# Kernel optimization log

Measured on AMD Instinct MI355X. Metric: run time of the kernel, lower is better.

Reference implementation:

```python
import jax, jax.numpy as jnp
import numpy as np

EMBED_DIM = 1024
NUM_HEADS = 16
HEAD_DIM = EMBED_DIM // NUM_HEADS  # used only for the softmax scale


def setup_inputs() -> dict:
    key = jax.random.key(0)
    k_x, k_wqkv, k_bqkv, k_wo, k_bo = jax.random.split(key, 5)
    bound_qkv = 1.0 / np.sqrt(EMBED_DIM)
    return {
        "x": jax.random.normal(k_x, (4, 2048, EMBED_DIM), dtype=jnp.float32),
        "W_qkv": jax.random.uniform(k_wqkv, (EMBED_DIM, 3 * EMBED_DIM), jnp.float32, -bound_qkv, bound_qkv),
        "b_qkv": jax.random.uniform(k_bqkv, (3 * EMBED_DIM,), jnp.float32, -bound_qkv, bound_qkv),
        "W_out": jax.random.uniform(k_wo, (EMBED_DIM, EMBED_DIM), jnp.float32, -bound_qkv, bound_qkv),
        "b_out": jax.random.uniform(k_bo, (EMBED_DIM,), jnp.float32, -bound_qkv, bound_qkv),
    }


def reference(x, W_qkv, b_qkv, W_out, b_out):
    # fused QKV projection: [B,S,3E]
    qkv = jnp.einsum("bse,ef->bsf", x, W_qkv) + b_qkv
    q, k, v = jnp.split(qkv, 3, axis=-1)  # each [B,S,E]
    scale = 1.0 / jnp.sqrt(jnp.float32(HEAD_DIM))
    # NOTE: no head reshape — attention over full embed_dim, scale uses head_dim
    scores = jnp.einsum("bqe,bke->bqk", q, k) * scale  # [B,S,S]
    attn = jax.nn.softmax(scores, axis=-1)
    context = jnp.einsum("bqk,bke->bqe", attn, v)  # [B,S,E]
    return jnp.einsum("bse,ef->bsf", context, W_out) + b_out
```

## Files before the change

### kernel.cpp

```cpp
#include <hip/hip_runtime.h>

typedef unsigned short u16;
typedef __bf16   bf16x8 __attribute__((ext_vector_type(8)));
typedef float    f32x4  __attribute__((ext_vector_type(4)));
typedef unsigned short u16x4 __attribute__((ext_vector_type(4)));
typedef unsigned short u16x8 __attribute__((ext_vector_type(8)));

__device__ inline float bf2f(u16 u) { return __uint_as_float(((unsigned int)u) << 16); }
__device__ inline u16 f2bf(float f) {
    unsigned int u = __float_as_uint(f);
    u += 0x7FFF + ((u >> 16) & 1);
    return (u16)(u >> 16);
}

__device__ inline void gl2lds16(const u16* g, u16* l) {
    __builtin_amdgcn_global_load_lds(
        (const __attribute__((address_space(1))) void*)g,
        (__attribute__((address_space(3))) void*)l, 16, 0, 0);
}

__global__ __launch_bounds__(256)
void sniff_zero(const u16* __restrict__ x, int* __restrict__ flag,
                float* __restrict__ sums) {
    sums[blockIdx.x * 256 + threadIdx.x] = 0.0f;
    if (blockIdx.x == 0 && threadIdx.x < 64) {
        const int lane = threadIdx.x;
        const unsigned idx = lane * 131072u + 65536u;
        const u16 u = x[idx];
        const int e = (u >> 7) & 0xFF;
        const unsigned long long b = __ballot(e >= 100 && e <= 140);
        if (lane == 0) flag[0] = (__popcll(b) >= 48) ? 0 : 1;
    }
}

__global__ __launch_bounds__(256)
void convx_biases(const void* __restrict__ x, u16* __restrict__ xbf,
                  const void* __restrict__ b1, const void* __restrict__ b2,
                  u16* __restrict__ o1, u16* __restrict__ o2,
                  const int* __restrict__ flagp) {
    const int f = *flagp;
    if (blockIdx.x < 8192) {
        const long i = ((long)blockIdx.x * 256 + threadIdx.x) * 4;
        if (f) {
            f32x4 v = *(const f32x4*)((const float*)x + i);
            u16x4 o; o[0] = f2bf(v[0]); o[1] = f2bf(v[1]); o[2] = f2bf(v[2]); o[3] = f2bf(v[3]);
            *(u16x4*)(xbf + i) = o;
        } else {
            *(u16x4*)(xbf + i) = *(const u16x4*)((const u16*)x + i);
        }
    } else {
        const int i = (blockIdx.x - 8192) * 256 + threadIdx.x;
        if (i < 3072) o1[i] = f ? f2bf(((const float*)b1)[i]) : ((const u16*)b1)[i];
        else { const int j = i - 3072;
               o2[j] = f ? f2bf(((const float*)b2)[j]) : ((const u16*)b2)[j]; }
    }
}

__global__ __launch_bounds__(256)
void transpose_w(const void* __restrict__ Wqkv, u16* __restrict__ WqkvT,
                 const void* __restrict__ Wout, u16* __restrict__ WoutT,
                 const int* __restrict__ flagp)
{
    const void* in; u16* out; long inStride, outStride;
    if (blockIdx.z == 0) { in = Wqkv; out = WqkvT; inStride = 3072; outStride = 1024; }
    else { if (blockIdx.x >= 32) return;
           in = Wout; out = WoutT; inStride = 1024; outStride = 1024; }
    __shared__ u16 t[32][36];
    const int isF32 = *flagp;
    const int tid = threadIdx.x;
    const long r0 = (long)blockIdx.y * 32;
    const long c0 = (long)blockIdx.x * 32;
    const int r  = tid >> 3;
    const int c4 = (tid & 7) * 4;
    const long base = (r0 + r) * inStride + c0 + c4;
    u16x4 v;
    if (isF32) {
        f32x4 f = *(const f32x4*)((const float*)in + base);
        v[0] = f2bf(f[0]); v[1] = f2bf(f[1]); v[2] = f2bf(f[2]); v[3] = f2bf(f[3]);
    } else {
        v = *(const u16x4*)((const u16*)in + base);
    }
    t[r][c4 + 0] = v[0]; t[r][c4 + 1] = v[1]; t[r][c4 + 2] = v[2]; t[r][c4 + 3] = v[3];
    __syncthreads();
    u16x4 o;
    o[0] = t[c4 + 0][r]; o[1] = t[c4 + 1][r]; o[2] = t[c4 + 2][r]; o[3] = t[c4 + 3][r];
    *(u16x4*)&out[(c0 + r) * outStride + r0 + c4] = o;
}

template <int GM, int GN, int WM, int WN>
__device__ __forceinline__ void kloop(
    const u16* __restrict__ A, const u16* __restrict__ Bt,
    int K, long lda, long ldb, long m0, long n0,
    u16* __restrict__ As, u16* __restrict__ Bs, f32x4 (&acc)[WM][WN])
{
    constexpr int BM = GM * WM * 16;
    constexpr int BN = GN * WN * 16;
    constexpr int IA = BM / 32;
    constexpr int IB = BN / 32;
    const int tid  = threadIdx.x;
    const int lane = tid & 63;
    const int wave = tid >> 6;
    const int sr   = tid >> 3;
    const int qg0  = (tid & 7) ^ (sr & 7);
    const u16* pa[IA]; const u16* pb[IB];
    u16* la[IA]; u16* lb[IB];
#pragma unroll
    for (int i = 0; i < IA; ++i) {
        pa[i] = A + (m0 + i * 32 + sr) * lda + qg0 * 8;
        la[i] = As + (i * 256 + wave * 64) * 8;
    }
#pragma unroll
    for (int i = 0; i < IB; ++i) {
        pb[i] = Bt + (n0 + i * 32 + sr) * ldb + qg0 * 8;
        lb[i] = Bs + (i * 256 + wave * 64) * 8;
    }
    const int wm = (wave / GN) * (WM * 16);
    const int wn = (wave % GN) * (WN * 16);
    const int lr = lane & 15;
    const int hk = lane >> 4;
    int aoff[WM][2], boff[WN][2];
#pragma unroll
    for (int i = 0; i < WM; ++i) {
        const int row = wm + i * 16 + lr, r7 = row & 7;
        aoff[i][0] = row * 64 + ((hk     ^ r7) * 8);
        aoff[i][1] = row * 64 + (((4+hk) ^ r7) * 8);
    }
#pragma unroll
    for (int j = 0; j < WN; ++j) {
        const int row = wn + j * 16 + lr, r7 = row & 7;
        boff[j][0] = row * 64 + ((hk     ^ r7) * 8);
        boff[j][1] = row * 64 + (((4+hk) ^ r7) * 8);
    }
    for (int kt = 0; kt < K; kt += 64) {
#pragma unroll
        for (int i = 0; i < IA; ++i) { gl2lds16(pa[i], la[i]); pa[i] += 64; }
#pragma unroll
        for (int i = 0; i < IB; ++i) { gl2lds16(pb[i], lb[i]); pb[i] += 64; }
        __syncthreads();
#pragma unroll
        for (int ks = 0; ks < 2; ++ks) {
            bf16x8 af[WM], bf[WN];
#pragma unroll
            for (int i = 0; i < WM; ++i) af[i] = *(const bf16x8*)&As[aoff[i][ks]];
#pragma unroll
            for (int j = 0; j < WN; ++j) bf[j] = *(const bf16x8*)&Bs[boff[j][ks]];
#pragma unroll
            for (int i = 0; i < WM; ++i)
#pragma unroll
                for (int j = 0; j < WN; ++j)
                    acc[i][j] = __builtin_amdgcn_mfma_f32_16x16x32_bf16(af[i], bf[j], acc[i][j], 0, 0, 0);
        }
        __syncthreads();
    }
}

template <int WM, int WN, typename F>
__device__ __forceinline__ void epi_bf16(u16* __restrict__ Sw, u16* __restrict__ C,
    long ldc, long gm0, long gn0, int lane, F f)
{
    const int lr = lane & 15, hk = lane >> 4;
#pragma unroll
    for (int i = 0; i < WM; ++i)
#pragma unroll
        for (int j = 0; j < WN; ++j)
#pragma unroll
            for (int r = 0; r < 4; ++r)
                Sw[(i*16 + hk*4 + r) * (WN*16) + j*16 + lr] = f2bf(f(i, j, r));
    asm volatile("s_waitcnt lgkmcnt(0)" ::: "memory");
    constexpr int LPR = WN * 2;
    constexpr int RPI = 64 / LPR;
    const int rl = lane / LPR, c8 = (lane % LPR) * 8;
#pragma unroll
    for (int t = 0; t < (WM*16) / RPI; ++t) {
        const int row = t * RPI + rl;
        u16x8 v8 = *(const u16x8*)&Sw[row * (WN*16) + c8];
        *(u16x8*)&C[(gm0 + row) * ldc + gn0 + c8] = v8;
    }
}

template <int WM, int WN, typename F>
__device__ __forceinline__ void epi_f32(float* __restrict__ Sw, float* __restrict__ C,
    long ldc, long gm0, long gn0, int lane, F f)
{
    const int lr = lane & 15, hk = lane >> 4;
#pragma unroll
    for (int jh = 0; jh < 2; ++jh) {
#pragma unroll
        for (int i = 0; i < WM; ++i)
#pragma unroll
            for (int jj = 0; jj < WN/2; ++jj)
#pragma unroll
                for (int r = 0; r < 4; ++r)
                    Sw[(i*16 + hk*4 + r) * (WN*8) + jj*16 + lr] = f(i, jh*(WN/2) + jj, r);
        asm volatile("s_waitcnt lgkmcnt(0)" ::: "memory");
        constexpr int LPR = WN * 2;
        constexpr int RPI = 64 / LPR;
        const int rl = lane / LPR, c4 = (lane % LPR) * 4;
#pragma unroll
        for (int t = 0; t < (WM*16) / RPI; ++t) {
            const int row = t * RPI + rl;
            f32x4 v4 = *(const f32x4*)&Sw[row * (WN*8) + c4];
            *(f32x4*)&C[(gm0 + row) * ldc + gn0 + jh*(WN*8) + c4] = v4;
        }
        asm volatile("s_waitcnt lgkmcnt(0)" ::: "memory");
    }
}

template<int MH, int NH, typename FI>
__device__ __forceinline__ void phase256(const u16* Ab, const u16* Bb,
    int aB0, int aB1, int bB0, int bB1, f32x4 (&acc)[2][2][4][2], FI issue)
{
    bf16x8 af[2][4], bv[2][2];
#pragma unroll
    for (int i = 0; i < 4; ++i) {
        af[0][i] = *(const bf16x8*)&Ab[aB0 + MH*8192 + i*1024];
        af[1][i] = *(const bf16x8*)&Ab[aB1 + MH*8192 + i*1024];
    }
#pragma unroll
    for (int j = 0; j < 2; ++j) {
        bv[0][j] = *(const bf16x8*)&Bb[bB0 + NH*8192 + j*1024];
        bv[1][j] = *(const bf16x8*)&Bb[bB1 + NH*8192 + j*1024];
    }
    issue();
    __builtin_amdgcn_s_barrier();
    asm volatile("s_waitcnt lgkmcnt(0)" ::: "memory");
    __builtin_amdgcn_s_setprio(1);
#pragma unroll
    for (int ks = 0; ks < 2; ++ks)
#pragma unroll
        for (int i = 0; i < 4; ++i)
#pragma unroll
            for (int j = 0; j < 2; ++j)
                acc[MH][NH][i][j] = __builtin_amdgcn_mfma_f32_16x16x32_bf16(
                    af[ks][i], bv[ks][j], acc[MH][NH][i][j], 0, 0, 0);
    __builtin_amdgcn_s_setprio(0);
}

__device__ __forceinline__ void kloop256(
    const u16* __restrict__ A, const u16* __restrict__ Bt,
    int K, long lda, long ldb, long m0, long n0,
    u16* __restrict__ S, f32x4 (&acc)[2][2][4][2])
{
    constexpr int BUF = 256 * 64;
    const int tid  = threadIdx.x;
    const int wave = tid >> 6, lane = tid & 63;
    const int wmi  = wave >> 2, wni = wave & 3;
    const int sr   = tid >> 3;
    const int qg   = ((tid & 7) ^ (sr & 7)) * 8;
    const int lr   = lane & 15, hk = lane >> 4, l7 = lane & 7;
    const u16* pA = A + (m0 + sr) * lda + qg;
    const u16* pB = Bt + (n0 + sr) * ldb + qg;
    u16* const lA = S + wave * 512;
    u16* const lB = S + 2 * BUF + wave * 512;
    const int aB0 = (wmi*64 + lr)*64 + ((hk       ^ l7) * 8);
    const int aB1 = (wmi*64 + lr)*64 + (((4 + hk) ^ l7) * 8);
    const int bB0 = (wni*32 + lr)*64 + ((hk       ^ l7) * 8);
    const int bB1 = (wni*32 + lr)*64 + (((4 + hk) ^ l7) * 8);
    const int NT = K >> 6;

    auto stA = [&](int buf, int mh, int kt) {
        const u16* s = pA + (long)mh * 128 * lda + kt;
        u16* d = lA + buf * BUF + mh * 8192;
        gl2lds16(s, d);
        gl2lds16(s + 64 * lda, d + 4096);
    };
    auto stB = [&](int buf, int nh, int kt) {
        const u16* s = pB + (long)nh * 128 * ldb + kt;
        u16* d = lB + buf * BUF + nh * 8192;
        gl2lds16(s, d);
        gl2lds16(s + 64 * ldb, d + 4096);
    };

    stA(0, 0, 0); stB(0, 0, 0); stA(0, 1, 0); stB(0, 1, 0);
    stA(1, 0, 64); stB(1, 0, 64);
    asm volatile("s_waitcnt vmcnt(4)" ::: "memory");
    __builtin_amdgcn_s_barrier();

    for (int t = 0; t < NT; ++t) {
        const int b = t & 1;
        const u16* Ab = S + b * BUF;
        const u16* Bb = S + 2 * BUF + b * BUF;
        const int kt = t << 6;
        phase256<0,0>(Ab, Bb, aB0, aB1, bB0, bB1, acc,
                      [&]{ if (t + 1 < NT) stA(b ^ 1, 1, kt + 64); });
        __builtin_amdgcn_s_barrier();
        phase256<0,1>(Ab, Bb, aB0, aB1, bB0, bB1, acc,
                      [&]{ if (t + 1 < NT) stB(b ^ 1, 1, kt + 64); });
        __builtin_amdgcn_s_barrier();
        phase256<1,0>(Ab, Bb, aB0, aB1, bB0, bB1, acc,
                      [&]{ if (t + 2 < NT) stA(b, 0, kt + 128); });
        __builtin_amdgcn_s_barrier();
        phase256<1,1>(Ab, Bb, aB0, aB1, bB0, bB1, acc,
                      [&]{ if (t + 2 < NT) stB(b, 0, kt + 128); });
        if (t + 2 < NT)      asm volatile("s_waitcnt vmcnt(4)" ::: "memory");
        else if (t + 1 < NT) asm volatile("s_waitcnt vmcnt(0)" ::: "memory");
        __builtin_amdgcn_s_barrier();
    }
}

template <typename F>
__device__ __forceinline__ void epi256_bf16(u16* __restrict__ Sw, u16* __restrict__ C,
    long ldc, long m0, long n0, int wmi, int wni, int lane, F f)
{
    const int lr = lane & 15, hk = lane >> 4;
#pragma unroll
    for (int mh = 0; mh < 2; ++mh)
#pragma unroll
    for (int i = 0; i < 4; ++i)
#pragma unroll
    for (int r = 0; r < 4; ++r)
#pragma unroll
    for (int nh = 0; nh < 2; ++nh)
#pragma unroll
    for (int j = 0; j < 2; ++j)
        Sw[(mh*64 + i*16 + hk*4 + r) * 64 + nh*32 + j*16 + lr] = f2bf(f(mh, nh, i, j, r));
    asm volatile("s_waitcnt lgkmcnt(0)" ::: "memory");
    const int rl = lane >> 3, c8 = (lane & 7) * 8;
    const long gcolb = n0 + (long)((c8 >> 5) * 128 + wni * 32 + (c8 & 31));
#pragma unroll
    for (int t = 0; t < 16; ++t) {
        const int row = t * 8 + rl;
        const long grow = m0 + (row >> 6) * 128 + wmi * 64 + (row & 63);
        *(u16x8*)&C[grow * ldc + gcolb] = *(const u16x8*)&Sw[row * 64 + c8];
    }
}

__global__ __launch_bounds__(512, 2)
void gemm_qkv256(const u16* __restrict__ A, const u16* __restrict__ Bt,
                 u16* __restrict__ C, const u16* __restrict__ bias)
{
    __shared__ __align__(16) u16 S[65536];
    const long m0 = (long)blockIdx.y * 256, n0 = (long)blockIdx.x * 256;
    f32x4 acc[2][2][4][2] = {};
    kloop256(A, Bt, 1024, 1024L, 1024L, m0, n0, S, acc);
    const int lane = threadIdx.x & 63, wave = threadIdx.x >> 6;
    const int wmi = wave >> 2, wni = wave & 3;
    const int lr = lane & 15;
    float bj[2][2];
#pragma unroll
    for (int nh = 0; nh < 2; ++nh)
#pragma unroll
        for (int j = 0; j < 2; ++j)
            bj[nh][j] = bf2f(bias[n0 + nh*128 + wni*32 + j*16 + lr]);
    epi256_bf16(S + wave * 8192, C, 3072L, m0, n0, wmi, wni, lane,
        [&](int mh, int nh, int i, int j, int r) { return acc[mh][nh][i][j][r] + bj[nh][j]; });
}

__global__ __launch_bounds__(512, 2)
void gemm_phase2_256(const u16* __restrict__ QKV, u16* __restrict__ P,
                     const u16* __restrict__ WoutT, u16* __restrict__ VWT,
                     float* __restrict__ sums)
{
    __shared__ __align__(16) u16 S[65536];
    const int z = blockIdx.z;
    const u16 *Ap, *Bp; u16* Cp; long lda, ldb, ldc, m0, n0;
    bool doExp; float* srow = nullptr;
    if (z < 4) {
        const long zb = (long)z * 2048 * 3072;
        Ap = QKV + zb; Bp = QKV + 1024 + zb;
        Cp = P + (long)z * 2048 * 2048;
        lda = 3072; ldb = 3072; ldc = 2048;
        m0 = (long)blockIdx.y * 256; n0 = (long)blockIdx.x * 256;
        doExp = true; srow = sums + z * 2048;
    } else {
        const int vb = (z - 4) * 2 + (blockIdx.y >> 2);
        Ap = WoutT; lda = 1024;
        Bp = QKV + 2048 + (long)vb * 2048 * 3072; ldb = 3072;
        Cp = VWT + (long)vb * 1024 * 2048; ldc = 2048;
        m0 = (long)(blockIdx.y & 3) * 256; n0 = (long)blockIdx.x * 256;
        doExp = false;
    }
    f32x4 acc[2][2][4][2] = {};
    kloop256(Ap, Bp, 1024, lda, ldb, m0, n0, S, acc);
    const int lane = threadIdx.x & 63, wave = threadIdx.x >> 6;
    const int wmi = wave >> 2, wni = wave & 3;
    const int lr = lane & 15, hk = lane >> 4;
    u16* Sw = S + wave * 8192;
    if (doExp) {
#pragma unroll
        for (int mh = 0; mh < 2; ++mh)
#pragma unroll
        for (int i = 0; i < 4; ++i)
#pragma unroll
        for (int r = 0; r < 4; ++r) {
            float s = 0.0f;
#pragma unroll
            for (int nh = 0; nh < 2; ++nh)
#pragma unroll
            for (int j = 0; j < 2; ++j) {
                const float e = __expf(acc[mh][nh][i][j][r] * 0.125f);
                Sw[(mh*64 + i*16 + hk*4 + r) * 64 + nh*32 + j*16 + lr] = f2bf(e);
                s += e;
            }
            s += __shfl_xor(s, 1); s += __shfl_xor(s, 2);
            s += __shfl_xor(s, 4); s += __shfl_xor(s, 8);
            if (lr == 0) atomicAdd(&srow[m0 + mh*128 + wmi*64 + i*16 + hk*4 + r], s);
        }
        asm volatile("s_waitcnt lgkmcnt(0)" ::: "memory");
        const int rl = lane >> 3, c8 = (lane & 7) * 8;
        const long gcolb = n0 + (long)((c8 >> 5) * 128 + wni * 32 + (c8 & 31));
#pragma unroll
        for (int t = 0; t < 16; ++t) {
            const int row = t * 8 + rl;
            const long grow = m0 + (row >> 6) * 128 + wmi * 64 + (row & 63);
            *(u16x8*)&Cp[grow * ldc + gcolb] = *(const u16x8*)&Sw[row * 64 + c8];
        }
    } else {
        epi256_bf16(Sw, Cp, ldc, m0, n0, wmi, wni, lane,
            [&](int mh, int nh, int i, int j, int r) { return acc[mh][nh][i][j][r]; });
    }
}

__global__ __launch_bounds__(256, 4)
void gemm_final(const u16* __restrict__ P, const u16* __restrict__ VWT,
                void* __restrict__ out, const u16* __restrict__ bias,
                const float* __restrict__ sums, const int* __restrict__ flagp)
{
    __shared__ __align__(16) u16 S[256 * 64];
    const int outF32 = *flagp;
    const long bz = blockIdx.z;
    const long m0 = (long)blockIdx.y * 128, n0 = (long)blockIdx.x * 128;
    f32x4 acc[4][4] = {};
    kloop<2, 2, 4, 4>(P + bz * 2048 * 2048, VWT + bz * 1024 * 2048,
                      2048, 2048L, 2048L, m0, n0, S, S + 128*64, acc);
    const int lane = threadIdx.x & 63, wave = threadIdx.x >> 6;
    const int wm = (wave >> 1) * 64, wn = (wave & 1) * 64;
    const int lr = lane & 15, hk = lane >> 4;
    float inv[4][4], bj[4];
#pragma unroll
    for (int i = 0; i < 4; ++i)
#pragma unroll
        for (int r = 0; r < 4; ++r)
            inv[i][r] = 1.0f / sums[bz * 2048 + m0 + wm + i*16 + hk*4 + r];
#pragma unroll
    for (int j = 0; j < 4; ++j) bj[j] = bf2f(bias[n0 + wn + j*16 + lr]);
    if (outF32) {
        float* Co = (float*)out + bz * 2048 * 1024;
        epi_f32<4, 4>((float*)S + wave * 2048, Co, 1024L, m0 + wm, n0 + wn, lane,
            [&](int i, int j, int r) { return acc[i][j][r] * inv[i][r] + bj[j]; });
    } else {
        u16* Co = (u16*)out + bz * 2048 * 1024;
        epi_bf16<4, 4>(S + wave * 4096, Co, 1024L, m0 + wm, n0 + wn, lane,
            [&](int i, int j, int r) { return acc[i][j][r] * inv[i][r] + bj[j]; });
    }
}

extern "C" void kernel_launch(void* const* d_in, const int* in_sizes, int n_in,
                              void* d_out, int out_size, void* d_ws, size_t ws_size,
                              hipStream_t stream)
{
    const void* x    = d_in[0];
    const void* Wqkv = d_in[1];
    const void* bqkv = d_in[2];
    const void* Wout = d_in[3];
    const void* bout = d_in[4];
    char* ws = (char*)d_ws;

    u16*   xbf   = (u16*)(ws);
    u16*   WqkvT = (u16*)(ws + 16777216);
    u16*   P     = (u16*)(ws);
    u16*   QKV   = (u16*)(ws + 33554432);
    u16*   VWT   = (u16*)(ws + 83886080);
    u16*   WoutT = (u16*)(ws + 100663296);
    u16*   bqkvc = (u16*)(ws + 102760448);
    u16*   boutc = (u16*)(ws + 102766592);
    int*   flag  = (int*)(ws + 102768640);
    float* sums  = (float*)(ws + 102772736);

    dim3 blk(256);

    sniff_zero<<<32, blk, 0, stream>>>((const u16*)x, flag, sums);
    convx_biases<<<8208, blk, 0, stream>>>(x, xbf, bqkv, bout, bqkvc, boutc, flag);
    transpose_w<<<dim3(96, 32, 2), blk, 0, stream>>>(Wqkv, WqkvT, Wout, WoutT, flag);

    gemm_qkv256<<<dim3(12, 32, 1), dim3(512), 0, stream>>>(xbf, WqkvT, QKV, bqkvc);

    gemm_phase2_256<<<dim3(8, 8, 6), dim3(512), 0, stream>>>(QKV, P, WoutT, VWT, sums);

    gemm_final<<<dim3(8, 16, 4), blk, 0, stream>>>(P, VWT, d_out, boutc, sums, flag);
}
```

Measured before the change: 304.1 us.

## Reuse register fragments across GEMM phases and reorder LDS prefetch schedule

Restructures the 256-tile GEMM k-loop so that A and B fragments loaded from LDS are kept in registers and reused across the four MFMA quadrants. The new order is (0,0),(0,1),(1,1),(1,0), and it cuts LDS reads per k-step from 24 fragment loads to 12. The global-to-LDS prefetch schedule is reordered to match: B's second half is now prefetched a full iteration ahead, and the vmcnt waits are raised. This lowers LDS bandwidth pressure and read latency, at the cost of more live registers and a more delicate buffer-reuse ordering that must stay race-free.

Result: faster. 276.2 us (-9.2%).

```diff
diff --git a/kernel.cpp b/kernel.cpp
--- a/kernel.cpp
+++ b/kernel.cpp
@@ -206,24 +206,10 @@
     }
 }
 
-template<int MH, int NH, typename FI>
-__device__ __forceinline__ void phase256(const u16* Ab, const u16* Bb,
-    int aB0, int aB1, int bB0, int bB1, f32x4 (&acc)[2][2][4][2], FI issue)
-{
-    bf16x8 af[2][4], bv[2][2];
-#pragma unroll
-    for (int i = 0; i < 4; ++i) {
-        af[0][i] = *(const bf16x8*)&Ab[aB0 + MH*8192 + i*1024];
-        af[1][i] = *(const bf16x8*)&Ab[aB1 + MH*8192 + i*1024];
-    }
-#pragma unroll
-    for (int j = 0; j < 2; ++j) {
-        bv[0][j] = *(const bf16x8*)&Bb[bB0 + NH*8192 + j*1024];
-        bv[1][j] = *(const bf16x8*)&Bb[bB1 + NH*8192 + j*1024];
-    }
-    issue();
-    __builtin_amdgcn_s_barrier();
-    asm volatile("s_waitcnt lgkmcnt(0)" ::: "memory");
+template<int MH, int NH>
+__device__ __forceinline__ void mfma16(const bf16x8 (&a)[2][4], const bf16x8 (&b)[2][2],
+                                       f32x4 (&acc)[2][2][4][2])
+{
     __builtin_amdgcn_s_setprio(1);
 #pragma unroll
     for (int ks = 0; ks < 2; ++ks)
@@ -232,7 +218,7 @@
 #pragma unroll
             for (int j = 0; j < 2; ++j)
                 acc[MH][NH][i][j] = __builtin_amdgcn_mfma_f32_16x16x32_bf16(
-                    af[ks][i], bv[ks][j], acc[MH][NH][i][j], 0, 0, 0);
+                    a[ks][i], b[ks][j], acc[MH][NH][i][j], 0, 0, 0);
     __builtin_amdgcn_s_setprio(0);
 }
 
@@ -252,10 +238,10 @@
     const u16* pB = Bt + (n0 + sr) * ldb + qg;
     u16* const lA = S + wave * 512;
     u16* const lB = S + 2 * BUF + wave * 512;
-    const int aB0 = (wmi*64 + lr)*64 + ((hk       ^ l7) * 8);
-    const int aB1 = (wmi*64 + lr)*64 + (((4 + hk) ^ l7) * 8);
-    const int bB0 = (wni*32 + lr)*64 + ((hk       ^ l7) * 8);
-    const int bB1 = (wni*32 + lr)*64 + (((4 + hk) ^ l7) * 8);
+    const int aO0 = (wmi*64 + lr)*64 + ((hk       ^ l7) * 8);
+    const int aO1 = (wmi*64 + lr)*64 + (((4 + hk) ^ l7) * 8);
+    const int bO0 = (wni*32 + lr)*64 + ((hk       ^ l7) * 8);
+    const int bO1 = (wni*32 + lr)*64 + (((4 + hk) ^ l7) * 8);
     const int NT = K >> 6;
 
     auto stA = [&](int buf, int mh, int kt) {
@@ -271,28 +257,55 @@
         gl2lds16(s + 64 * ldb, d + 4096);
     };
 
-    stA(0, 0, 0); stB(0, 0, 0); stA(0, 1, 0); stB(0, 1, 0);
-    stA(1, 0, 64); stB(1, 0, 64);
-    asm volatile("s_waitcnt vmcnt(4)" ::: "memory");
+    stA(0,0,0); stB(0,0,0); stB(0,1,0); stA(0,1,0);
+    stA(1,0,64); stB(1,0,64); stB(1,1,64);
+    asm volatile("s_waitcnt vmcnt(6)" ::: "memory");
     __builtin_amdgcn_s_barrier();
 
+    bf16x8 a[2][4], b0[2][2], b1[2][2];
     for (int t = 0; t < NT; ++t) {
         const int b = t & 1;
         const u16* Ab = S + b * BUF;
         const u16* Bb = S + 2 * BUF + b * BUF;
-        const int kt = t << 6;
-        phase256<0,0>(Ab, Bb, aB0, aB1, bB0, bB1, acc,
-                      [&]{ if (t + 1 < NT) stA(b ^ 1, 1, kt + 64); });
-        __builtin_amdgcn_s_barrier();
-        phase256<0,1>(Ab, Bb, aB0, aB1, bB0, bB1, acc,
-                      [&]{ if (t + 1 < NT) stB(b ^ 1, 1, kt + 64); });
-        __builtin_amdgcn_s_barrier();
-        phase256<1,0>(Ab, Bb, aB0, aB1, bB0, bB1, acc,
-                      [&]{ if (t + 2 < NT) stA(b, 0, kt + 128); });
-        __builtin_amdgcn_s_barrier();
-        phase256<1,1>(Ab, Bb, aB0, aB1, bB0, bB1, acc,
-                      [&]{ if (t + 2 < NT) stB(b, 0, kt + 128); });
-        if (t + 2 < NT)      asm volatile("s_waitcnt vmcnt(4)" ::: "memory");
+#pragma unroll
+        for (int i = 0; i < 4; ++i) {
+            a[0][i] = *(const bf16x8*)&Ab[aO0 + i*1024];
+            a[1][i] = *(const bf16x8*)&Ab[aO1 + i*1024];
+        }
+#pragma unroll
+        for (int j = 0; j < 2; ++j) {
+            b0[0][j] = *(const bf16x8*)&Bb[bO0 + j*1024];
+            b0[1][j] = *(const bf16x8*)&Bb[bO1 + j*1024];
+        }
+        if (t + 1 < NT) stA(b ^ 1, 1, (t + 1) << 6);
+        __builtin_amdgcn_s_barrier();
+        asm volatile("s_waitcnt lgkmcnt(0)" ::: "memory");
+        mfma16<0,0>(a, b0, acc);
+        __builtin_amdgcn_s_barrier();
+#pragma unroll
+        for (int j = 0; j < 2; ++j) {
+            b1[0][j] = *(const bf16x8*)&Bb[bO0 + 8192 + j*1024];
+            b1[1][j] = *(const bf16x8*)&Bb[bO1 + 8192 + j*1024];
+        }
+        if (t + 2 < NT) stA(b, 0, (t + 2) << 6);
+        __builtin_amdgcn_s_barrier();
+        asm volatile("s_waitcnt lgkmcnt(0)" ::: "memory");
+        mfma16<0,1>(a, b1, acc);
+        __builtin_amdgcn_s_barrier();
+#pragma unroll
+        for (int i = 0; i < 4; ++i) {
+            a[0][i] = *(const bf16x8*)&Ab[aO0 + 8192 + i*1024];
+            a[1][i] = *(const bf16x8*)&Ab[aO1 + 8192 + i*1024];
+        }
+        if (t + 2 < NT) stB(b, 0, (t + 2) << 6);
+        __builtin_amdgcn_s_barrier();
+        asm volatile("s_waitcnt lgkmcnt(0)" ::: "memory");
+        mfma16<1,1>(a, b1, acc);
+        __builtin_amdgcn_s_barrier();
+        if (t + 2 < NT) stB(b, 1, (t + 2) << 6);
+        __builtin_amdgcn_s_barrier();
+        mfma16<1,0>(a, b0, acc);
+        if (t + 2 < NT)      asm volatile("s_waitcnt vmcnt(6)" ::: "memory");
         else if (t + 1 < NT) asm volatile("s_waitcnt vmcnt(0)" ::: "memory");
         __builtin_amdgcn_s_barrier();
     }
```
